# Optimization experiments

Hardware: AMD Instinct MI355X
Metric: run time of the kernel (lower is better)

Reference implementation:

```python
import jax, jax.numpy as jnp
import numpy as np

D = 128          # embed_dim
V = 200000       # num_symbols (pad idx = V)
B = 4096         # query batch
BS = 1           # support batch (one-shot)
M = 50           # max neighbors
STEPS = 4        # process_steps
DM = 2 * D       # d_model = 256
H = 2 * DM       # LSTM hidden = 512
EPS = 1e-3       # LayerNormalization eps in source repo


def setup_inputs() -> dict:
    key = jax.random.key(0)
    ks = jax.random.split(key, 32)
    nrm = lambda k, s: jax.random.normal(k, s, jnp.float32) * 0.05
    ri = lambda k, s, hi: jax.random.randint(k, s, 0, hi)
    emb = nrm(ks[0], (V + 1, D)).at[V].set(0.0)  # padding_idx row zeroed
    return {
        "query": ri(ks[1], (B, 2), V),
        "support": ri(ks[2], (BS, 2), V),
        "q_l1": ri(ks[3], (B, M, 2), V + 1),
        "q_l2": ri(ks[4], (B, M, 2), V + 1),
        "q_deg_l": ri(ks[5], (B,), M),
        "q_r1": ri(ks[6], (B, M, 2), V + 1),
        "q_r2": ri(ks[7], (B, M, 2), V + 1),
        "q_deg_r": ri(ks[8], (B,), M),
        "s_l1": ri(ks[9], (BS, M, 2), V + 1),
        "s_l2": ri(ks[10], (BS, M, 2), V + 1),
        "s_deg_l": ri(ks[11], (BS,), M),
        "s_r1": ri(ks[12], (BS, M, 2), V + 1),
        "s_r2": ri(ks[13], (BS, M, 2), V + 1),
        "s_deg_r": ri(ks[14], (BS,), M),
        "emb": emb,
        "gcn_W": nrm(ks[15], (D, 2 * D)),
        "gcn_lb": jnp.zeros(D, jnp.float32),   # nn.Linear bias of gcn_w
        "gcn_b": jnp.zeros(D, jnp.float32),    # extra gcn_b parameter
        "attn_W": nrm(ks[16], (1, D)),
        "attn_b": jnp.zeros(1, jnp.float32),
        "gate_W": nrm(ks[17], (1, D)),
        "gate_lb": jnp.zeros(1, jnp.float32),   # nn.Linear bias of gate_w
        "gate_b": jnp.zeros(1, jnp.float32),    # extra gate_b parameter
        "p1_W": nrm(ks[18], (2 * DM, DM)),
        "p1_b": jnp.zeros(2 * DM, jnp.float32),
        "p2_W": nrm(ks[19], (DM, 2 * DM)),
        "p2_b": jnp.zeros(DM, jnp.float32),
        "ln_a": jnp.ones(DM, jnp.float32),
        "ln_b": jnp.zeros(DM, jnp.float32),
        "Wih": nrm(ks[20], (4 * H, DM)),
        "Whh": nrm(ks[21], (4 * H, H)),
        "bih": jnp.zeros(4 * H, jnp.float32),
        "bhh": jnp.zeros(4 * H, jnp.float32),
    }


def reference(query, support, q_l1, q_l2, q_deg_l, q_r1, q_r2, q_deg_r,
              s_l1, s_l2, s_deg_l, s_r1, s_r2, s_deg_r,
              emb, gcn_W, gcn_lb, gcn_b, attn_W, attn_b,
              gate_W, gate_lb, gate_b, p1_W, p1_b, p2_W, p2_b,
              ln_a, ln_b, Wih, Whh, bih, bhh):
    # dropout is identity (eval / p=0). deg tensors are unused, as in source.

    def nbr(conn, self_ids):
        # conn: [b, M, 2] -> gather rel/ent embeddings, project, attend, gate
        rel = emb[conn[:, :, 0]]            # [b, M, D]
        ent = emb[conn[:, :, 1]]            # [b, M, D]
        x = jnp.concatenate([rel, ent], axis=-1)             # [b, M, 2D]
        proj = jnp.einsum('bmc,dc->bmd', x, gcn_W) + gcn_lb + gcn_b
        proj = jnp.where(proj >= 0, proj, 0.01 * proj)        # leaky_relu
        scores = jnp.einsum('bmd,od->bmo', proj, attn_W) + attn_b  # [b, M, 1]
        w = jax.nn.softmax(scores, axis=1)
        agg = jnp.sum(proj * w, axis=1)                       # [b, D]
        gate = jax.nn.sigmoid(agg @ gate_W.T + gate_lb + gate_b)  # [b, 1]
        return gate * agg + (1.0 - gate) * emb[self_ids]

    def pair_vec(h_ids, t_ids, l1, l2, r1, r2):
        left = (nbr(l1, h_ids) + nbr(l2, h_ids)) / 2.0
        right = (nbr(r1, t_ids) + nbr(r2, t_ids)) / 2.0
        return jnp.concatenate([left, right], axis=-1)        # [b, 2D]

    qv = pair_vec(query[:, 0], query[:, 1], q_l1, q_l2, q_r1, q_r2)   # [B, DM]
    sv = pair_vec(support[:, 0], support[:, 1], s_l1, s_l2, s_r1, s_r2)  # [BS, DM]

    # SupportEncoder: FFN + residual + LayerNormalization (std w/ Bessel, eps=1e-3)
    h = jax.nn.relu(sv @ p1_W.T + p1_b) @ p2_W.T + p2_b + sv
    mu = h.mean(-1, keepdims=True)
    sig = jnp.std(h, axis=-1, keepdims=True, ddof=1)
    sg = (h - mu) / (sig + EPS) * ln_a + ln_b                 # [BS, DM]

    # QueryEncoder: process-attention LSTM (torch LSTMCell gate order i,f,g,o)
    def step(carry, _):
        hq, h_r, c = carry
        g = qv @ Wih.T + bih + h_r @ Whh.T + bhh
        i, f, gg, o = jnp.split(g, 4, axis=-1)
        c = jax.nn.sigmoid(f) * c + jax.nn.sigmoid(i) * jnp.tanh(gg)
        hh = jax.nn.sigmoid(o) * jnp.tanh(c)
        hq = qv + hh[:, :DM]
        a = jax.nn.softmax(hq @ sg.T, axis=1)                 # [B, BS]
        r = a @ sg                                            # [B, DM]
        return (hq, jnp.concatenate([hq, r], axis=1), c), None

    z = jnp.zeros((qv.shape[0], H), qv.dtype)
    (qg, _, _), _ = jax.lax.scan(step, (qv, z, z), None, length=STEPS)

    return jnp.sum(qg * sg, axis=1)                           # [B]
```

## Files before the change

kernel.cpp:

```cpp
#include <hip/hip_runtime.h>

#define D    128
#define VSZ  200000
#define NB   4096
#define MM   50
#define DM   256
#define HSZ  512
#define G4   2048

typedef __attribute__((ext_vector_type(8))) short short8;
typedef __attribute__((ext_vector_type(4))) float floatx4;

__device__ __forceinline__ float sigf(float x) { return 1.0f / (1.0f + __expf(-x)); }
__device__ __forceinline__ float tanhfast(float x) { return 1.0f - 2.0f / (__expf(2.0f * x) + 1.0f); }
__device__ __forceinline__ unsigned short f2bf(float x) {
    unsigned int u = __float_as_uint(x);
    u += 0x7FFFu + ((u >> 16) & 1u);
    return (unsigned short)(u >> 16);
}
__device__ __forceinline__ float bf2f(unsigned short s) {
    return __uint_as_float(((unsigned int)s) << 16);
}

__device__ __forceinline__ void async_copy16(void* lds, const void* gsrc) {
    __builtin_amdgcn_global_load_lds(
        (const __attribute__((address_space(1))) unsigned int*)gsrc,
        (__attribute__((address_space(3))) unsigned int*)lds, 16, 0, 0);
}

__global__ __launch_bounds__(256) void k_pack(
    const float* __restrict__ Wih, const float* __restrict__ Whh,
    const float* __restrict__ bih, const float* __restrict__ bhh,
    const float* __restrict__ gcn_W,
    unsigned short* __restrict__ Wihp, unsigned short* __restrict__ Whhp,
    float* __restrict__ gb, unsigned short* __restrict__ Wb)
{
    int idx = blockIdx.x * 256 + threadIdx.x;
    if (idx < 131072) {
        int ci = idx & 65535;
        int lane = ci & 63, rest = ci >> 6;
        int ks = rest & 7, tile = rest >> 3;
        int n = tile * 16 + (lane & 15), k = ks * 32 + (lane >> 4) * 8;
        const float* src = (idx < 65536) ? (Wih + (size_t)n * 256 + k)
                                         : (Whh + (size_t)n * 512 + k);
        unsigned short* dst = (idx < 65536) ? Wihp : Whhp;
        short8 o;
        #pragma unroll
        for (int j = 0; j < 8; ++j) o[j] = (short)f2bf(src[j]);
        *(short8*)(dst + (size_t)ci * 8) = o;
    } else if (idx < 131072 + 2048) {
        int i = idx - 131072;
        gb[i] = bih[i] + bhh[i];
    } else if (idx < 131072 + 2048 + 32768) {
        int i = idx - (131072 + 2048);
        int n = i >> 7, k = i & 127;
        float v = (n < 128) ? gcn_W[n * 256 + k] : gcn_W[(n - 128) * 256 + 128 + k];
        Wb[i] = f2bf(v);
    }
}

__global__ __launch_bounds__(256, 4) void k_proj_mfma(
    const float* __restrict__ emb, const unsigned short* __restrict__ Wb,
    const float* __restrict__ gcn_lb, const float* __restrict__ gcn_b,
    unsigned short* __restrict__ P1, unsigned short* __restrict__ P2, int nrows)
{
    __shared__ unsigned short S[16896];
    int t = threadIdx.x;
    int v0 = blockIdx.x * 64;
    int lane = t & 63, w = t >> 6;
    int nl = lane & 15, quad = lane >> 4;
    int n0 = w * 64;

    #pragma unroll
    for (int it = 0; it < 8; ++it) {
        int chunk = w * 8 + it;
        int o = chunk * 1024 + lane * 16;
        int row = o >> 9;
        int b = o & 511;
        int bs = b ^ ((row & 7) << 5);
        int v = v0 + row;
        v = (v < nrows) ? v : (nrows - 1);
        async_copy16((char*)S + chunk * 1024,
                     (const char*)emb + (size_t)v * 512 + bs);
    }
    __syncthreads();

    floatx4 acc[4][4];
    #pragma unroll
    for (int mt = 0; mt < 4; ++mt)
        #pragma unroll
        for (int nt = 0; nt < 4; ++nt)
            acc[mt][nt] = (floatx4){0.f, 0.f, 0.f, 0.f};

    const char* Sb = (const char*)S;
    #pragma unroll
    for (int ks = 0; ks < 4; ++ks) {
        short8 bfr[4];
        #pragma unroll
        for (int nt = 0; nt < 4; ++nt)
            bfr[nt] = *(const short8*)(Wb + (size_t)(n0 + nt * 16 + nl) * 128 + ks * 32 + quad * 8);
        short8 af[4];
        #pragma unroll
        for (int mt = 0; mt < 4; ++mt) {
            int row = mt * 16 + nl;
            int b = ks * 128 + quad * 32;
            int ba = row * 512 + (b ^ ((row & 7) << 5));
            float4 lo = *(const float4*)(Sb + ba);
            float4 hi = *(const float4*)(Sb + ba + 16);
            short8 a;
            a[0] = (short)f2bf(lo.x); a[1] = (short)f2bf(lo.y);
            a[2] = (short)f2bf(lo.z); a[3] = (short)f2bf(lo.w);
            a[4] = (short)f2bf(hi.x); a[5] = (short)f2bf(hi.y);
            a[6] = (short)f2bf(hi.z); a[7] = (short)f2bf(hi.w);
            af[mt] = a;
        }
        #pragma unroll
        for (int mt = 0; mt < 4; ++mt)
            #pragma unroll
            for (int nt = 0; nt < 4; ++nt)
                acc[mt][nt] = __builtin_amdgcn_mfma_f32_16x16x32_bf16(
                    af[mt], bfr[nt], acc[mt][nt], 0, 0, 0);
    }

    __syncthreads();
    #pragma unroll
    for (int nt = 0; nt < 4; ++nt) {
        int col = n0 + nt * 16 + nl;
        float bias = (col < 128) ? (gcn_lb[col] + gcn_b[col]) : 0.f;
        #pragma unroll
        for (int mt = 0; mt < 4; ++mt)
            #pragma unroll
            for (int reg = 0; reg < 4; ++reg)
                S[(mt * 16 + quad * 4 + reg) * 264 + col] =
                    f2bf(acc[mt][nt][reg] + bias);
    }
    __syncthreads();
    #pragma unroll
    for (int it = 0; it < 8; ++it) {
        int c = t + 256 * it;
        int row = c >> 5, c8 = c & 31;
        int v = v0 + row;
        if (v < nrows) {
            int4 val = *(const int4*)(S + row * 264 + c8 * 8);
            unsigned short* dst = (c8 < 16) ? (P1 + (size_t)v * D + c8 * 8)
                                            : (P2 + (size_t)v * D + (c8 - 16) * 8);
            *(int4*)dst = val;
        }
    }
}

__global__ __launch_bounds__(256) void k_nbr(
    const int* __restrict__ query, const int* __restrict__ support,
    const int* __restrict__ q_l1, const int* __restrict__ q_l2,
    const int* __restrict__ q_r1, const int* __restrict__ q_r2,
    const int* __restrict__ s_l1, const int* __restrict__ s_l2,
    const int* __restrict__ s_r1, const int* __restrict__ s_r2,
    const unsigned short* __restrict__ P1, const unsigned short* __restrict__ P2,
    const float* __restrict__ emb,
    const float* __restrict__ attn_W, const float* __restrict__ attn_b,
    const float* __restrict__ gate_W, const float* __restrict__ gate_lb,
    const float* __restrict__ gate_b,
    float* __restrict__ qv, unsigned short* __restrict__ qvbf,
    float* __restrict__ sv)
{
    __shared__ unsigned short proj[2 * MM * 136];
    __shared__ int rel[2 * MM], ent[2 * MM];
    __shared__ float scw[2 * 64];
    __shared__ float scp[2][2][64];
    __shared__ float aw[D], gw[D];
    __shared__ float redg[4];
    __shared__ float gateS[2];
    __shared__ float oth[D];

    int bid = blockIdx.x;
    int item = bid >> 1;
    int side = bid & 1;
    int t = threadIdx.x;

    const int* cA; const int* cB; int selfid; float* outp; bool isq;
    if (item < NB) {
        isq = true;
        cA = (side ? q_r1 : q_l1) + (size_t)item * MM * 2;
        cB = (side ? q_r2 : q_l2) + (size_t)item * MM * 2;
        selfid = query[item * 2 + side];
        outp = qv + (size_t)item * DM + side * D;
    } else {
        isq = false;
        int i2 = item - NB;
        cA = (side ? s_r1 : s_l1) + (size_t)i2 * MM * 2;
        cB = (side ? s_r2 : s_l2) + (size_t)i2 * MM * 2;
        selfid = support[i2 * 2 + side];
        outp = sv + (size_t)i2 * DM + side * D;
    }
    if (t < D) { aw[t] = attn_W[t]; gw[t] = gate_W[t]; }
    if (t < 2 * MM) {
        const int* c = (t < MM) ? cA : cB;
        int m = (t < MM) ? t : t - MM;
        rel[t] = c[m * 2]; ent[t] = c[m * 2 + 1];
    }
    __syncthreads();
    for (int e8 = t; e8 < 2 * MM * 16; e8 += 256) {
        int m = e8 >> 4, d8 = (e8 & 15) * 8;
        short8 a = *(const short8*)(P1 + (size_t)rel[m] * D + d8);
        short8 b = *(const short8*)(P2 + (size_t)ent[m] * D + d8);
        short8 o;
        #pragma unroll
        for (int j = 0; j < 8; ++j) {
            float p = bf2f((unsigned short)a[j]) + bf2f((unsigned short)b[j]);
            p = (p >= 0.f) ? p : 0.01f * p;
            o[j] = (short)f2bf(p);
        }
        *(short8*)(proj + m * 136 + d8) = o;
    }
    __syncthreads();
    {
        int tab = t >> 7, g = (t >> 6) & 1, m = t & 63;
        float s = 0.f;
        if (m < MM) {
            const unsigned short* pr = proj + (tab * MM + m) * 136 + g * 64;
            #pragma unroll
            for (int i = 0; i < 8; ++i) {
                short8 v8 = *(const short8*)(pr + i * 8);
                #pragma unroll
                for (int j = 0; j < 8; ++j)
                    s += bf2f((unsigned short)v8[j]) * aw[g * 64 + i * 8 + j];
            }
        }
        scp[tab][g][m] = s;
    }
    __syncthreads();
    if (t < 128) {
        int tab = t >> 6, m = t & 63;
        float v = (m < MM) ? (scp[tab][0][m] + scp[tab][1][m] + attn_b[0]) : -1e30f;
        float mx = v;
        #pragma unroll
        for (int o = 32; o > 0; o >>= 1) mx = fmaxf(mx, __shfl_xor(mx, o, 64));
        float ev = (m < MM) ? __expf(v - mx) : 0.f;
        float sm = ev;
        #pragma unroll
        for (int o = 32; o > 0; o >>= 1) sm += __shfl_xor(sm, o, 64);
        if (m < MM) scw[tab * 64 + m] = ev / sm;
    }
    __syncthreads();
    int tab = t >> 7, d = t & 127;
    float agg = 0.f;
    #pragma unroll 5
    for (int m = 0; m < MM; ++m)
        agg += scw[tab * 64 + m] * bf2f(proj[(tab * MM + m) * 136 + d]);
    float gpart = agg * gw[d];
    #pragma unroll
    for (int o = 32; o > 0; o >>= 1) gpart += __shfl_xor(gpart, o, 64);
    if ((t & 63) == 0) redg[t >> 6] = gpart;
    __syncthreads();
    if (t == 0)  gateS[0] = sigf(redg[0] + redg[1] + gate_lb[0] + gate_b[0]);
    if (t == 64) gateS[1] = sigf(redg[2] + redg[3] + gate_lb[0] + gate_b[0]);
    __syncthreads();
    float embd = emb[(size_t)selfid * D + d];
    float val = gateS[tab] * agg + (1.f - gateS[tab]) * embd;
    if (tab == 1) oth[d] = val;
    __syncthreads();
    if (tab == 0) {
        float r = 0.5f * (val + oth[d]);
        outp[d] = r;
        if (isq) qvbf[(size_t)item * DM + side * D + d] = f2bf(r);
    }
}

__global__ __launch_bounds__(256) void k_sg1(
    const float* __restrict__ sv, const float* __restrict__ p1_W,
    const float* __restrict__ p1_b, float* __restrict__ hid)
{
    __shared__ float s[DM];
    int t = threadIdx.x;
    s[t] = sv[t];
    __syncthreads();
    int j = blockIdx.x * 32 + (t >> 3);
    int pp = t & 7;
    const float* w = p1_W + (size_t)j * DM + pp * 32;
    float a = 0.f;
    #pragma unroll
    for (int i = 0; i < 8; ++i) {
        float4 v = *(const float4*)(w + i * 4);
        int c = pp * 32 + i * 4;
        a += v.x * s[c] + v.y * s[c + 1] + v.z * s[c + 2] + v.w * s[c + 3];
    }
    a += __shfl_xor(a, 1, 64);
    a += __shfl_xor(a, 2, 64);
    a += __shfl_xor(a, 4, 64);
    if (pp == 0) hid[j] = fmaxf(a + p1_b[j], 0.f);
}

__global__ __launch_bounds__(256) void k_sg2(
    const float* __restrict__ sv, const float* __restrict__ hid,
    const float* __restrict__ p2_W, const float* __restrict__ p2_b,
    float* __restrict__ h)
{
    __shared__ float hs[2 * DM];
    int t = threadIdx.x;
    hs[t] = hid[t]; hs[t + 256] = hid[t + 256];
    __syncthreads();
    int r = blockIdx.x * 32 + (t >> 3);
    int pp = t & 7;
    const float* w = p2_W + (size_t)r * (2 * DM) + pp * 64;
    float a = 0.f;
    #pragma unroll
    for (int i = 0; i < 16; ++i) {
        float4 v = *(const float4*)(w + i * 4);
        int c = pp * 64 + i * 4;
        a += v.x * hs[c] + v.y * hs[c + 1] + v.z * hs[c + 2] + v.w * hs[c + 3];
    }
    a += __shfl_xor(a, 1, 64);
    a += __shfl_xor(a, 2, 64);
    a += __shfl_xor(a, 4, 64);
    if (pp == 0) h[r] = a + p2_b[r] + sv[r];
}

__global__ __launch_bounds__(256) void k_sg3(
    const float* __restrict__ h, const float* __restrict__ ln_a,
    const float* __restrict__ ln_b, float* __restrict__ sg)
{
    __shared__ float red[8];
    int t = threadIdx.x;
    float x = h[t];
    float sm = x;
    #pragma unroll
    for (int o = 32; o > 0; o >>= 1) sm += __shfl_xor(sm, o, 64);
    if ((t & 63) == 0) red[t >> 6] = sm;
    __syncthreads();
    float mu = (red[0] + red[1] + red[2] + red[3]) * (1.0f / 256.0f);
    float dv = x - mu;
    float sq = dv * dv;
    #pragma unroll
    for (int o = 32; o > 0; o >>= 1) sq += __shfl_xor(sq, o, 64);
    if ((t & 63) == 0) red[4 + (t >> 6)] = sq;
    __syncthreads();
    float var = (red[4] + red[5] + red[6] + red[7]) * (1.0f / 255.0f);
    float sig = sqrtf(var);
    sg[t] = dv / (sig + 0.001f) * ln_a[t] + ln_b[t];
}

__global__ __launch_bounds__(256) void k_sgwhh(
    const float* __restrict__ sg, const float* __restrict__ Whh,
    float* __restrict__ sgW)
{
    __shared__ float s[DM];
    int t = threadIdx.x;
    s[t] = sg[t];
    __syncthreads();
    int k = blockIdx.x * 64 + (t >> 2);
    int pp = t & 3;
    const float* w = Whh + (size_t)k * HSZ + DM + pp * 64;
    float a = 0.f;
    #pragma unroll
    for (int i = 0; i < 16; ++i) {
        float4 v = *(const float4*)(w + i * 4);
        int c = pp * 64 + i * 4;
        a += v.x * s[c] + v.y * s[c + 1] + v.z * s[c + 2] + v.w * s[c + 3];
    }
    a += __shfl_xor(a, 1, 64);
    a += __shfl_xor(a, 2, 64);
    if (pp == 0) sgW[k] = a;
}

__global__ __launch_bounds__(512, 2) void k_lstm_fused(
    const float* __restrict__ qv, const unsigned short* __restrict__ qvbf,
    const unsigned short* __restrict__ Wihp, const unsigned short* __restrict__ Whhp,
    const float* __restrict__ gb, const float* __restrict__ sgW,
    const float* __restrict__ sg, float* __restrict__ out)
{
    __shared__ unsigned short Ab[16 * 264];
    __shared__ float redbuf[8][16];
    int t = threadIdx.x;
    int lane = t & 63, w = t >> 6;
    int nl = lane & 15, quad = lane >> 4;
    int b0 = blockIdx.x * 16;

    {
        int row = t >> 5, c16 = t & 31;
        *(int4*)(Ab + row * 264 + c16 * 8) =
            *(const int4*)(qvbf + (size_t)(b0 + row) * DM + c16 * 8);
    }
    int kt[2] = { w, w + 8 };

    float sgWreg[2][4], qvreg[2][4], sgreg2[2];
    float cc[2][4];
    ushort4 g0s[2][4];
    #pragma unroll
    for (int j = 0; j < 2; ++j) {
        #pragma unroll
        for (int g = 0; g < 4; ++g)
            sgWreg[j][g] = sgW[g * 512 + kt[j] * 16 + nl];
        sgreg2[j] = sg[kt[j] * 16 + nl];
        #pragma unroll
        for (int r = 0; r < 4; ++r)
            qvreg[j][r] = qv[(size_t)(b0 + quad * 4 + r) * DM + kt[j] * 16 + nl];
    }
    __syncthreads();

    #pragma unroll 1
    for (int st = 0; st < 3; ++st) {
        short8 af[8];
        #pragma unroll
        for (int ks = 0; ks < 8; ++ks)
            af[ks] = *(const short8*)(Ab + nl * 264 + ks * 32 + quad * 8);
        const unsigned short* Bp = (st == 0) ? Wihp : Whhp;
        floatx4 acc[2][4];
        #pragma unroll
        for (int j = 0; j < 2; ++j)
            #pragma unroll
            for (int g = 0; g < 4; ++g)
                acc[j][g] = (floatx4){0.f, 0.f, 0.f, 0.f};
        #pragma unroll
        for (int j = 0; j < 2; ++j)
            #pragma unroll
            for (int g = 0; g < 4; ++g) {
                int T = g * 32 + kt[j];
                #pragma unroll
                for (int ks = 0; ks < 8; ++ks) {
                    short8 bfr = *(const short8*)(Bp + ((size_t)(T * 8 + ks) * 64 + lane) * 8);
                    acc[j][g] = __builtin_amdgcn_mfma_f32_16x16x32_bf16(
                        af[ks], bfr, acc[j][g], 0, 0, 0);
                }
            }
        float hval[2][4];
        if (st == 0) {
            #pragma unroll
            for (int j = 0; j < 2; ++j) {
                float bi  = gb[0 * 512 + kt[j] * 16 + nl];
                float bf_ = gb[1 * 512 + kt[j] * 16 + nl];
                float bg  = gb[2 * 512 + kt[j] * 16 + nl];
                float bo  = gb[3 * 512 + kt[j] * 16 + nl];
                #pragma unroll
                for (int r = 0; r < 4; ++r) {
                    float gi_ = acc[j][0][r] + bi;
                    float gf_ = acc[j][1][r] + bf_;
                    float gg_ = acc[j][2][r] + bg;
                    float go_ = acc[j][3][r] + bo;
                    ((unsigned short*)&g0s[j][0])[r] = f2bf(gi_);
                    ((unsigned short*)&g0s[j][1])[r] = f2bf(gf_);
                    ((unsigned short*)&g0s[j][2])[r] = f2bf(gg_);
                    ((unsigned short*)&g0s[j][3])[r] = f2bf(go_);
                    float cn = sigf(gi_) * tanhfast(gg_);
                    cc[j][r] = cn;
                    hval[j][r] = qvreg[j][r] + sigf(go_) * tanhfast(cn);
                }
            }
        } else {
            #pragma unroll
            for (int j = 0; j < 2; ++j)
                #pragma unroll
                for (int r = 0; r < 4; ++r) {
                    float gi_ = acc[j][0][r] + sgWreg[j][0] + bf2f(((unsigned short*)&g0s[j][0])[r]);
                    float gf_ = acc[j][1][r] + sgWreg[j][1] + bf2f(((unsigned short*)&g0s[j][1])[r]);
                    float gg_ = acc[j][2][r] + sgWreg[j][2] + bf2f(((unsigned short*)&g0s[j][2])[r]);
                    float go_ = acc[j][3][r] + sgWreg[j][3] + bf2f(((unsigned short*)&g0s[j][3])[r]);
                    float cn = sigf(gf_) * cc[j][r] + sigf(gi_) * tanhfast(gg_);
                    cc[j][r] = cn;
                    hval[j][r] = qvreg[j][r] + sigf(go_) * tanhfast(cn);
                }
        }
        __syncthreads();
        #pragma unroll
        for (int j = 0; j < 2; ++j)
            #pragma unroll
            for (int r = 0; r < 4; ++r)
                Ab[(quad * 4 + r) * 264 + kt[j] * 16 + nl] = f2bf(hval[j][r]);
        __syncthreads();
    }

    {
        short8 af[8];
        #pragma unroll
        for (int ks = 0; ks < 8; ++ks)
            af[ks] = *(const short8*)(Ab + nl * 264 + ks * 32 + quad * 8);
        floatx4 acc[2][4];
        #pragma unroll
        for (int j = 0; j < 2; ++j)
            #pragma unroll
            for (int g = 0; g < 4; ++g)
                acc[j][g] = (floatx4){0.f, 0.f, 0.f, 0.f};
        #pragma unroll
        for (int j = 0; j < 2; ++j)
            #pragma unroll
            for (int g = 0; g < 4; ++g) {
                int T = g * 32 + kt[j];
                #pragma unroll
                for (int ks = 0; ks < 8; ++ks) {
                    short8 bfr = *(const short8*)(Whhp + ((size_t)(T * 8 + ks) * 64 + lane) * 8);
                    acc[j][g] = __builtin_amdgcn_mfma_f32_16x16x32_bf16(
                        af[ks], bfr, acc[j][g], 0, 0, 0);
                }
            }
        float part[4] = {0.f, 0.f, 0.f, 0.f};
        #pragma unroll
        for (int j = 0; j < 2; ++j)
            #pragma unroll
            for (int r = 0; r < 4; ++r) {
                float gi_ = acc[j][0][r] + sgWreg[j][0] + bf2f(((unsigned short*)&g0s[j][0])[r]);
                float gf_ = acc[j][1][r] + sgWreg[j][1] + bf2f(((unsigned short*)&g0s[j][1])[r]);
                float gg_ = acc[j][2][r] + sgWreg[j][2] + bf2f(((unsigned short*)&g0s[j][2])[r]);
                float go_ = acc[j][3][r] + sgWreg[j][3] + bf2f(((unsigned short*)&g0s[j][3])[r]);
                float cn = sigf(gf_) * cc[j][r] + sigf(gi_) * tanhfast(gg_);
                float h = qvreg[j][r] + sigf(go_) * tanhfast(cn);
                part[r] += h * sgreg2[j];
            }
        #pragma unroll
        for (int r = 0; r < 4; ++r) {
            float p = part[r];
            p += __shfl_xor(p, 1, 64);
            p += __shfl_xor(p, 2, 64);
            p += __shfl_xor(p, 4, 64);
            p += __shfl_xor(p, 8, 64);
            if (nl == 0) redbuf[w][quad * 4 + r] = p;
        }
    }
    __syncthreads();
    if (t < 16) {
        float s = 0.f;
        #pragma unroll
        for (int w2 = 0; w2 < 8; ++w2) s += redbuf[w2][t];
        out[b0 + t] = s;
    }
}

extern "C" void kernel_launch(void* const* d_in, const int* in_sizes, int n_in,
                              void* d_out, int out_size, void* d_ws, size_t ws_size,
                              hipStream_t stream) {
    const int* query   = (const int*)d_in[0];
    const int* support = (const int*)d_in[1];
    const int* q_l1 = (const int*)d_in[2];
    const int* q_l2 = (const int*)d_in[3];
    const int* q_r1 = (const int*)d_in[5];
    const int* q_r2 = (const int*)d_in[6];
    const int* s_l1 = (const int*)d_in[8];
    const int* s_l2 = (const int*)d_in[9];
    const int* s_r1 = (const int*)d_in[11];
    const int* s_r2 = (const int*)d_in[12];
    const float* emb    = (const float*)d_in[14];
    const float* gcn_W  = (const float*)d_in[15];
    const float* gcn_lb = (const float*)d_in[16];
    const float* gcn_b  = (const float*)d_in[17];
    const float* attn_W = (const float*)d_in[18];
    const float* attn_b = (const float*)d_in[19];
    const float* gate_W = (const float*)d_in[20];
    const float* gate_lb = (const float*)d_in[21];
    const float* gate_b  = (const float*)d_in[22];
    const float* p1_W = (const float*)d_in[23];
    const float* p1_b = (const float*)d_in[24];
    const float* p2_W = (const float*)d_in[25];
    const float* p2_b = (const float*)d_in[26];
    const float* ln_a = (const float*)d_in[27];
    const float* ln_b = (const float*)d_in[28];
    const float* Wih  = (const float*)d_in[29];
    const float* Whh  = (const float*)d_in[30];
    const float* bih  = (const float*)d_in[31];
    const float* bhh  = (const float*)d_in[32];

    unsigned short* P1   = (unsigned short*)d_ws;
    unsigned short* P2   = P1 + (size_t)(VSZ + 1) * D;
    unsigned short* Wb   = P2 + (size_t)(VSZ + 1) * D;
    unsigned short* Wihp = Wb + 256 * 128;
    unsigned short* Whhp = Wihp + (size_t)65536 * 8;
    unsigned short* qvbf = Whhp + (size_t)65536 * 8;
    float* fws = (float*)(qvbf + (size_t)NB * DM);
    float* gbv = fws;  fws += G4;
    float* qvb = fws;  fws += (size_t)NB * DM;
    float* svb = fws;  fws += DM;
    float* sgb = fws;  fws += DM;
    float* sgW = fws;  fws += G4 + 4;
    float* hidb = fws; fws += 2 * DM;
    float* hb  = fws;  fws += DM;
    (void)in_sizes; (void)n_in; (void)out_size; (void)ws_size;

    k_pack<<<648, 256, 0, stream>>>(
        Wih, Whh, bih, bhh, gcn_W, Wihp, Whhp, gbv, Wb);
    k_proj_mfma<<<(VSZ + 1 + 63) / 64, 256, 0, stream>>>(
        emb, Wb, gcn_lb, gcn_b, P1, P2, VSZ + 1);
    k_nbr<<<2 * (NB + 1), 256, 0, stream>>>(
        query, support, q_l1, q_l2, q_r1, q_r2, s_l1, s_l2, s_r1, s_r2,
        P1, P2, emb, attn_W, attn_b, gate_W, gate_lb, gate_b, qvb, qvbf, svb);
    k_sg1<<<16, 256, 0, stream>>>(svb, p1_W, p1_b, hidb);
    k_sg2<<<8, 256, 0, stream>>>(svb, hidb, p2_W, p2_b, hb);
    k_sg3<<<1, 256, 0, stream>>>(hb, ln_a, ln_b, sgb);
    k_sgwhh<<<32, 256, 0, stream>>>(sgb, Whh, sgW);
    k_lstm_fused<<<256, 512, 0, stream>>>(
        qvb, qvbf, Wihp, Whhp, gbv, sgW, sgb, (float*)d_out);
}
```

Before: 378.5 us.

## Make embedding projection kernel persistent with double-buffered async prefetch

```diff
diff --git a/kernel.cpp b/kernel.cpp
--- a/kernel.cpp
+++ b/kernel.cpp
@@ -59,93 +59,123 @@
     }
 }
 
-__global__ __launch_bounds__(256, 4) void k_proj_mfma(
+__global__ __launch_bounds__(256, 3) void k_proj_mfma(
     const float* __restrict__ emb, const unsigned short* __restrict__ Wb,
     const float* __restrict__ gcn_lb, const float* __restrict__ gcn_b,
     unsigned short* __restrict__ P1, unsigned short* __restrict__ P2, int nrows)
 {
-    __shared__ unsigned short S[16896];
+    __shared__ __align__(16) unsigned char Buf[2][16384];
+    __shared__ unsigned short C[32 * 264];
     int t = threadIdx.x;
-    int v0 = blockIdx.x * 64;
     int lane = t & 63, w = t >> 6;
     int nl = lane & 15, quad = lane >> 4;
     int n0 = w * 64;
-
-    #pragma unroll
-    for (int it = 0; it < 8; ++it) {
-        int chunk = w * 8 + it;
-        int o = chunk * 1024 + lane * 16;
-        int row = o >> 9;
-        int b = o & 511;
-        int bs = b ^ ((row & 7) << 5);
-        int v = v0 + row;
-        v = (v < nrows) ? v : (nrows - 1);
-        async_copy16((char*)S + chunk * 1024,
-                     (const char*)emb + (size_t)v * 512 + bs);
-    }
-    __syncthreads();
-
-    floatx4 acc[4][4];
-    #pragma unroll
-    for (int mt = 0; mt < 4; ++mt)
-        #pragma unroll
-        for (int nt = 0; nt < 4; ++nt)
-            acc[mt][nt] = (floatx4){0.f, 0.f, 0.f, 0.f};
-
-    const char* Sb = (const char*)S;
-    #pragma unroll
-    for (int ks = 0; ks < 4; ++ks) {
-        short8 bfr[4];
-        #pragma unroll
-        for (int nt = 0; nt < 4; ++nt)
-            bfr[nt] = *(const short8*)(Wb + (size_t)(n0 + nt * 16 + nl) * 128 + ks * 32 + quad * 8);
-        short8 af[4];
-        #pragma unroll
-        for (int mt = 0; mt < 4; ++mt) {
-            int row = mt * 16 + nl;
-            int b = ks * 128 + quad * 32;
-            int ba = row * 512 + (b ^ ((row & 7) << 5));
-            float4 lo = *(const float4*)(Sb + ba);
-            float4 hi = *(const float4*)(Sb + ba + 16);
-            short8 a;
-            a[0] = (short)f2bf(lo.x); a[1] = (short)f2bf(lo.y);
-            a[2] = (short)f2bf(lo.z); a[3] = (short)f2bf(lo.w);
-            a[4] = (short)f2bf(hi.x); a[5] = (short)f2bf(hi.y);
-            a[6] = (short)f2bf(hi.z); a[7] = (short)f2bf(hi.w);
-            af[mt] = a;
-        }
-        #pragma unroll
-        for (int mt = 0; mt < 4; ++mt)
+    int G = gridDim.x;
+    int ntile = (nrows + 31) >> 5;
+
+    auto STAGE = [&](int pb, int tile) {
+        int v0 = tile * 32;
+        #pragma unroll
+        for (int it = 0; it < 4; ++it) {
+            int chunk = w * 4 + it;
+            int o = chunk * 1024 + lane * 16;
+            int row = o >> 9;
+            int b = o & 511;
+            int bs = b ^ ((row & 7) << 5);
+            int v = v0 + row;
+            v = (v < nrows) ? v : (nrows - 1);
+            async_copy16(Buf[pb] + chunk * 1024,
+                         (const char*)emb + (size_t)v * 512 + bs);
+        }
+    };
+
+    short8 bfr[4][4];
+    #pragma unroll
+    for (int nt = 0; nt < 4; ++nt)
+        #pragma unroll
+        for (int ks = 0; ks < 4; ++ks)
+            bfr[nt][ks] = *(const short8*)(Wb + (size_t)(n0 + nt * 16 + nl) * 128 + ks * 32 + quad * 8);
+
+    STAGE(0, blockIdx.x);
+    int pb = 0;
+    bool first = true;
+    for (int tile = blockIdx.x; tile < ntile; tile += G) {
+        int nxt = tile + G;
+        bool pf = (nxt < ntile);
+        if (pf) STAGE(pb ^ 1, nxt);
+        if (first) {
+            if (pf) asm volatile("s_waitcnt vmcnt(4)" ::: "memory");
+            else    asm volatile("s_waitcnt vmcnt(0)" ::: "memory");
+        } else {
+            if (pf) asm volatile("s_waitcnt vmcnt(8)" ::: "memory");
+            else    asm volatile("s_waitcnt vmcnt(4)" ::: "memory");
+        }
+        __builtin_amdgcn_sched_barrier(0);
+        __builtin_amdgcn_s_barrier();
+        __builtin_amdgcn_sched_barrier(0);
+
+        floatx4 acc[2][4];
+        #pragma unroll
+        for (int mt = 0; mt < 2; ++mt)
             #pragma unroll
             for (int nt = 0; nt < 4; ++nt)
-                acc[mt][nt] = __builtin_amdgcn_mfma_f32_16x16x32_bf16(
-                    af[mt], bfr[nt], acc[mt][nt], 0, 0, 0);
-    }
-
-    __syncthreads();
-    #pragma unroll
-    for (int nt = 0; nt < 4; ++nt) {
-        int col = n0 + nt * 16 + nl;
-        float bias = (col < 128) ? (gcn_lb[col] + gcn_b[col]) : 0.f;
-        #pragma unroll
-        for (int mt = 0; mt < 4; ++mt)
-            #pragma unroll
-            for (int reg = 0; reg < 4; ++reg)
-                S[(mt * 16 + quad * 4 + reg) * 264 + col] =
-                    f2bf(acc[mt][nt][reg] + bias);
-    }
-    __syncthreads();
-    #pragma unroll
-    for (int it = 0; it < 8; ++it) {
-        int c = t + 256 * it;
-        int row = c >> 5, c8 = c & 31;
-        int v = v0 + row;
-        if (v < nrows) {
-            int4 val = *(const int4*)(S + row * 264 + c8 * 8);
-            unsigned short* dst = (c8 < 16) ? (P1 + (size_t)v * D + c8 * 8)
-                                            : (P2 + (size_t)v * D + (c8 - 16) * 8);
-            *(int4*)dst = val;
-        }
+                acc[mt][nt] = (floatx4){0.f, 0.f, 0.f, 0.f};
+        const char* Sb = (const char*)Buf[pb];
+        #pragma unroll
+        for (int ks = 0; ks < 4; ++ks) {
+            short8 af[2];
+            #pragma unroll
+            for (int mt = 0; mt < 2; ++mt) {
+                int row = mt * 16 + nl;
+                int b = ks * 128 + quad * 32;
+                int ba = row * 512 + (b ^ ((row & 7) << 5));
+                float4 lo = *(const float4*)(Sb + ba);
+                float4 hi = *(const float4*)(Sb + ba + 16);
+                short8 a;
+                a[0] = (short)f2bf(lo.x); a[1] = (short)f2bf(lo.y);
+                a[2] = (short)f2bf(lo.z); a[3] = (short)f2bf(lo.w);
+                a[4] = (short)f2bf(hi.x); a[5] = (short)f2bf(hi.y);
+                a[6] = (short)f2bf(hi.z); a[7] = (short)f2bf(hi.w);
+                af[mt] = a;
+            }
+            #pragma unroll
+            for (int mt = 0; mt < 2; ++mt)
+                #pragma unroll
+                for (int nt = 0; nt < 4; ++nt)
+                    acc[mt][nt] = __builtin_amdgcn_mfma_f32_16x16x32_bf16(
+                        af[mt], bfr[nt][ks], acc[mt][nt], 0, 0, 0);
+        }
+
+        #pragma unroll
+        for (int nt = 0; nt < 4; ++nt) {
+            int col = n0 + nt * 16 + nl;
+            float bias = (col < 128) ? (gcn_lb[col] + gcn_b[col]) : 0.f;
+            #pragma unroll
+            for (int mt = 0; mt < 2; ++mt)
+                #pragma unroll
+                for (int reg = 0; reg < 4; ++reg)
+                    C[(mt * 16 + quad * 4 + reg) * 264 + col] =
+                        f2bf(acc[mt][nt][reg] + bias);
+        }
+        asm volatile("s_waitcnt lgkmcnt(0)" ::: "memory");
+        __builtin_amdgcn_sched_barrier(0);
+        __builtin_amdgcn_s_barrier();
+        __builtin_amdgcn_sched_barrier(0);
+
+        #pragma unroll
+        for (int it = 0; it < 4; ++it) {
+            int c = t + 256 * it;
+            int row = c >> 5, c8 = c & 31;
+            int v = tile * 32 + row;
+            if (v < nrows) {
+                int4 val = *(const int4*)(C + row * 264 + c8 * 8);
+                unsigned short* dst = (c8 < 16) ? (P1 + (size_t)v * D + c8 * 8)
+                                                : (P2 + (size_t)v * D + (c8 - 16) * 8);
+                *(int4*)dst = val;
+            }
+        }
+        pb ^= 1;
+        first = false;
     }
 }
 
@@ -574,7 +604,7 @@
 
     k_pack<<<648, 256, 0, stream>>>(
         Wih, Whh, bih, bhh, gcn_W, Wihp, Whhp, gbv, Wb);
-    k_proj_mfma<<<(VSZ + 1 + 63) / 64, 256, 0, stream>>>(
+    k_proj_mfma<<<768, 256, 0, stream>>>(
         emb, Wb, gcn_lb, gcn_b, P1, P2, VSZ + 1);
     k_nbr<<<2 * (NB + 1), 256, 0, stream>>>(
         query, support, q_l1, q_l2, q_r1, q_r2, s_l1, s_l2, s_r1, s_r2,
```

New measurement: 360.1 us. 4.9% less time.
